# Kernel tuning notes

Hardware: AMD Instinct MI355X
Metric: run time of the kernel (lower is better)

Reference implementation:

```python
import jax, jax.numpy as jnp
import numpy as np
import math

KEY_DIM = 16
COMPAT_FACTOR = 1.0 / math.sqrt(KEY_DIM)


def setup_inputs() -> dict:
    key = jax.random.key(0)
    k1, k2, k3, k4, k5 = jax.random.split(key, 5)
    B, G, D, H, K, V = 4, 2048, 128, 8, 16, 16
    h = jax.random.normal(k1, (B, G, D), dtype=jnp.float32)
    # mask: 1 = masked-out (attention forced to zero), 0 = attend
    mask = jax.random.randint(k2, (G, G), 0, 2, dtype=jnp.int32)
    # xavier_uniform over (input_dim, key_dim) fan per head
    lim_qk = math.sqrt(6.0 / (D + K))
    lim_v = math.sqrt(6.0 / (D + V))
    W_Q = jax.random.uniform(k3, (H, D, K), jnp.float32, -lim_qk, lim_qk)
    W_K = jax.random.uniform(k4, (H, D, K), jnp.float32, -lim_qk, lim_qk)
    W_V = jax.random.uniform(k5, (H, D, V), jnp.float32, -lim_v, lim_v)
    return {"h": h, "mask": mask, "W_Q": W_Q, "W_K": W_K, "W_V": W_V}


def reference(h, mask, W_Q, W_K, W_V):
    # h: [B, G, D]; W_Q/W_K: [H, D, K]; W_V: [H, D, V]; mask: [G, G] (1 = masked)
    q = jnp.einsum("bgd,hdk->bhgk", h, W_Q)  # [B, H, G, K]
    k = jnp.einsum("bgd,hdk->bhgk", h, W_K)  # [B, H, G, K]
    v = jnp.einsum("bgd,hdv->bhgv", h, W_V)  # [B, H, G, V]
    compat = COMPAT_FACTOR * jnp.einsum("bhqk,bhgk->bhqg", q, k)  # [B, H, G, G]
    masked = (mask > 0)[None, None, :, :]  # broadcast over batch, heads
    neg = jnp.finfo(compat.dtype).min
    compat = jnp.where(masked, neg, compat)
    attn = jax.nn.softmax(compat, axis=-1)
    # post-softmax hard zeroing at masked positions (as in the original)
    attn = jnp.where(masked, jnp.zeros((), attn.dtype), attn)
    h_p = jnp.einsum("bhqg,bhgv->bhqv", attn, v)  # [B, H, G, V]
    return h_p
```

## Files before the change

### kernel.cpp

```cpp
#include <hip/hip_runtime.h>
#include <hip/hip_bf16.h>

#define GG 2048
#define DD 128
#define HH 8
#define BH 32

typedef _Float16 h2 __attribute__((ext_vector_type(2)));
typedef _Float16 h4 __attribute__((ext_vector_type(4)));
typedef _Float16 h8 __attribute__((ext_vector_type(8)));
typedef __attribute__((ext_vector_type(4))) float f32x4;
typedef unsigned short u16;
typedef unsigned int   u32;
typedef unsigned char  u8;
typedef unsigned long long u64;

#define QSCALE 0.36067376022224085f

#define OFF_Q  0u
#define OFF_KV (2u << 20)
#define OFF_M  (6u << 20)

#if __has_builtin(__builtin_amdgcn_exp2f)
#define EXP2F(x) __builtin_amdgcn_exp2f(x)
#else
#define EXP2F(x) exp2f(x)
#endif

#define MFMA16(a, b, c) __builtin_amdgcn_mfma_f32_16x16x16f16(a, b, c, 0, 0, 0)

static __device__ __forceinline__ u16 f16b(float x) {
  return __builtin_bit_cast(u16, (_Float16)x);
}

__global__ __launch_bounds__(256) void prep_kernel(
    const float* __restrict__ h, const int* __restrict__ mask,
    const float* __restrict__ WQ, const float* __restrict__ WK,
    const float* __restrict__ WV,
    _Float16* __restrict__ Qh, u8* __restrict__ KVp, u8* __restrict__ mbt)
{
  const int blk = blockIdx.x, tid = threadIdx.x;

  if (blk >= 256) {
    int t = (blk - 256) * 256 + tid;
    const int* m = mask + (size_t)t * 8;
    int4 m0 = *(const int4*)m;
    int4 m1 = *(const int4*)(m + 4);
    u32 byte = (m0.x > 0) | ((m0.y > 0) << 1) | ((m0.z > 0) << 2) | ((m0.w > 0) << 3)
             | ((m1.x > 0) << 4) | ((m1.y > 0) << 5) | ((m1.z > 0) << 6) | ((m1.w > 0) << 7);
    int q  = t >> 8;
    int k8 = t & 255;
    mbt[(size_t)(k8 >> 4) * (GG * 16) + (size_t)q * 16 + (k8 & 15)] = (u8)byte;
    return;
  }

  __shared__ _Float16 Wl[48 * 136];
  const int bh = blk >> 3, b = bh >> 3, hh = bh & (HH - 1);

  #pragma unroll
  for (int m = 0; m < 3; ++m) {
    const float* W = (m == 0 ? WQ : (m == 1 ? WK : WV)) + (size_t)hh * DD * 16;
    const float sc = (m == 0) ? QSCALE : 1.0f;
    #pragma unroll
    for (int i = 0; i < 2; ++i) {
      int j4 = i * 256 + tid;
      float4 v = ((const float4*)W)[j4];
      int j = j4 * 4, d = j >> 4, n0 = m * 16 + (j & 15);
      Wl[(n0 + 0) * 136 + d] = (_Float16)(v.x * sc);
      Wl[(n0 + 1) * 136 + d] = (_Float16)(v.y * sc);
      Wl[(n0 + 2) * 136 + d] = (_Float16)(v.z * sc);
      Wl[(n0 + 3) * 136 + d] = (_Float16)(v.w * sc);
    }
  }
  __syncthreads();

  const int wave = tid >> 6, lane = tid & 63;
  const int col = lane & 15, quad = lane >> 4;
  const int g0 = ((blk & 7) * 4 + wave) * 64;
  const float* hb = h + (size_t)b * GG * DD;

  f32x4 acc[4][3];
  #pragma unroll
  for (int mt = 0; mt < 4; ++mt)
    #pragma unroll
    for (int nt = 0; nt < 3; ++nt)
      acc[mt][nt] = (f32x4){0.f, 0.f, 0.f, 0.f};

  #pragma unroll
  for (int s = 0; s < 4; ++s) {
    h8 a[4], bw[3];
    #pragma unroll
    for (int mt = 0; mt < 4; ++mt) {
      const float* src = hb + (size_t)(g0 + mt * 16 + col) * DD + s * 32 + quad * 8;
      float4 x = ((const float4*)src)[0];
      float4 y = ((const float4*)src)[1];
      a[mt] = (h8){ (_Float16)x.x, (_Float16)x.y, (_Float16)x.z, (_Float16)x.w,
                    (_Float16)y.x, (_Float16)y.y, (_Float16)y.z, (_Float16)y.w };
    }
    #pragma unroll
    for (int nt = 0; nt < 3; ++nt)
      bw[nt] = *(const h8*)&Wl[(nt * 16 + col) * 136 + s * 32 + quad * 8];
    #pragma unroll
    for (int mt = 0; mt < 4; ++mt)
      #pragma unroll
      for (int nt = 0; nt < 3; ++nt)
        acc[mt][nt] = __builtin_amdgcn_mfma_f32_16x16x32_f16(a[mt], bw[nt], acc[mt][nt], 0, 0, 0);
  }

  u8* kvb = KVp + (size_t)bh * 16 * 8192;
  #pragma unroll
  for (int mt = 0; mt < 4; ++mt) {
    #pragma unroll
    for (int r = 0; r < 4; ++r) {
      int g = g0 + mt * 16 + quad * 4 + r;
      Qh[((size_t)bh * GG + g) * 16 + col] = (_Float16)acc[mt][0][r];
      int gi = g & 127;
      u8* tb = kvb + (size_t)(g >> 7) * 8192;
      *(u16*)(tb + gi * 32 + col * 2) = f16b(acc[mt][1][r]);
      *(u16*)(tb + 4096 + col * 256 + ((((gi >> 2) + col) & 31) * 8)
                 + (g & 3) * 2) = f16b(acc[mt][2][r]);
    }
  }
}

__global__ __launch_bounds__(512, 4) void attn_kernel(
    const _Float16* __restrict__ Qh, const u8* __restrict__ KVp,
    const u8* __restrict__ mbt, float* __restrict__ out)
{
  __shared__ __align__(16) u8 kv[2][16384];
  const int tid = threadIdx.x, wv = tid >> 6, lane = tid & 63;
  const int col = lane & 15, quad = lane >> 4;
  const int bh = blockIdx.x & 31;
  const int qb = (blockIdx.x >> 5) * 128 + wv * 16;

  const h4 qf = *(const h4*)(Qh + ((size_t)bh * GG + qb + col) * 16 + quad * 4);
  const u8* kvsrc = KVp + (size_t)bh * 16 * 8192;
  const u8* mrow  = mbt + (size_t)(qb + col) * 16;

  f32x4 acc = {0.f,0.f,0.f,0.f}, lacc = {0.f,0.f,0.f,0.f};
  const f32x4 cinit = {-4.f, -4.f, -4.f, -4.f};
  const h4 ones = {(_Float16)1.f, (_Float16)1.f, (_Float16)1.f, (_Float16)1.f};
  const int shq = quad * 4;

  auto tile = [&](const u8* cur, uint4 mv) {
    const _Float16* ldsK = (const _Float16*)cur;
    const u8* ldsV = cur + 4096;
    u64 w0 = ((u64)mv.x | ((u64)mv.y << 32)) >> shq;
    u64 w1 = ((u64)mv.z | ((u64)mv.w << 32)) >> shq;
    #pragma unroll
    for (int st = 0; st < 8; ++st) {
      h4 kf = *(const h4*)(ldsK + (size_t)(st * 16 + col) * 16 + quad * 4);
      h4 vf = *(const h4*)(ldsV + col * 256 + (((st * 4 + quad + col) & 31) * 8));

      f32x4 s = MFMA16(kf, qf, cinit);
      u32 bits = (u32)(((st < 4) ? w0 : w1) >> ((st & 3) * 16)) & 0xFu;
      float p0 = (bits & 1u) ? 0.f : EXP2F(s[0]);
      float p1 = (bits & 2u) ? 0.f : EXP2F(s[1]);
      float p2 = (bits & 4u) ? 0.f : EXP2F(s[2]);
      float p3 = (bits & 8u) ? 0.f : EXP2F(s[3]);

      h2 a01 = __builtin_bit_cast(h2, __builtin_amdgcn_cvt_pkrtz(p0, p1));
      h2 a23 = __builtin_bit_cast(h2, __builtin_amdgcn_cvt_pkrtz(p2, p3));
      h4 pf = __builtin_shufflevector(a01, a23, 0, 1, 2, 3);

      acc  = MFMA16(vf, pf, acc);
      lacc = MFMA16(ones, pf, lacc);
    }
  };

  {
    uint4 a0 = *(const uint4*)(kvsrc + tid * 32);
    uint4 a1 = *(const uint4*)(kvsrc + tid * 32 + 16);
    *(uint4*)(kv[0] + tid * 32) = a0;
    *(uint4*)(kv[0] + tid * 32 + 16) = a1;
  }
  uint4 mv0 = *(const uint4*)mrow;
  uint4 mv1 = *(const uint4*)(mrow + (size_t)(GG * 16));
  __syncthreads();

  for (int it = 0; it < 8; ++it) {
    uint4 na0, na1, nm0, nm1;
    if (it < 7) {
      const u8* ns = kvsrc + (size_t)(it + 1) * 16384 + tid * 32;
      na0 = *(const uint4*)ns;
      na1 = *(const uint4*)(ns + 16);
      nm0 = *(const uint4*)(mrow + (size_t)(2 * it + 2) * (GG * 16));
      nm1 = *(const uint4*)(mrow + (size_t)(2 * it + 3) * (GG * 16));
    }

    const u8* cur = kv[it & 1];
    tile(cur, mv0);
    tile(cur + 8192, mv1);

    if (it < 7) {
      u8* nb = kv[(it + 1) & 1];
      *(uint4*)(nb + tid * 32) = na0;
      *(uint4*)(nb + tid * 32 + 16) = na1;
      mv0 = nm0; mv1 = nm1;
      __syncthreads();
    }
  }

  const float l = lacc[0];
  const float rl = (l > 0.f) ? (1.f / l) : 0.f;
  float4 o = { acc[0] * rl, acc[1] * rl, acc[2] * rl, acc[3] * rl };
  *(float4*)(out + ((size_t)bh * GG + qb + col) * 16 + quad * 4) = o;
}

extern "C" void kernel_launch(void* const* d_in, const int* in_sizes, int n_in,
                              void* d_out, int out_size, void* d_ws, size_t ws_size,
                              hipStream_t stream) {
  const float* h    = (const float*)d_in[0];
  const int*   mask = (const int*)d_in[1];
  const float* WQ   = (const float*)d_in[2];
  const float* WK   = (const float*)d_in[3];
  const float* WV   = (const float*)d_in[4];
  float* out = (float*)d_out;
  char* ws = (char*)d_ws;
  _Float16* Qh  = (_Float16*)(ws + OFF_Q);
  u8*       KVp = (u8*)(ws + OFF_KV);
  u8*       mbt = (u8*)(ws + OFF_M);

  hipLaunchKernelGGL(prep_kernel, dim3(256 + GG * GG / (256 * 8)), dim3(256), 0, stream,
                     h, mask, WQ, WK, WV, Qh, KVp, mbt);
  hipLaunchKernelGGL(attn_kernel, dim3(BH * (GG / 128)), dim3(512), 0, stream,
                     Qh, KVp, mbt, out);
}
```

Before: 112.6 us.

## Split key range across wave halves with two query tiles per wave and LDS reduction

Each wave now handles 32 queries (two 16-row tiles) over half of the key range, and the two wave groups' partial numerators and denominators are combined through shared memory at the end. Each K/V fragment read from LDS is reused for two query tiles, which halves LDS reads per MFMA and gives more independent MFMA chains per wave. This adds LDS space for the reduction, an extra barrier, and more registers per thread, which may limit occupancy at the 512x4 launch bounds.

```diff
diff --git a/kernel.cpp b/kernel.cpp
--- a/kernel.cpp
+++ b/kernel.cpp
@@ -128,83 +128,127 @@
     const u8* __restrict__ mbt, float* __restrict__ out)
 {
   __shared__ __align__(16) u8 kv[2][16384];
+  __shared__ float Lacc[4][32][17];
+  __shared__ float Ll[4][32];
   const int tid = threadIdx.x, wv = tid >> 6, lane = tid & 63;
   const int col = lane & 15, quad = lane >> 4;
+  const int g  = wv & 3;
+  const int kh = wv >> 2;
   const int bh = blockIdx.x & 31;
-  const int qb = (blockIdx.x >> 5) * 128 + wv * 16;
-
-  const h4 qf = *(const h4*)(Qh + ((size_t)bh * GG + qb + col) * 16 + quad * 4);
+  const int qb = (blockIdx.x >> 5) * 128 + g * 32;
+
+  const h4 qf0 = *(const h4*)(Qh + ((size_t)bh * GG + qb + col) * 16 + quad * 4);
+  const h4 qf1 = *(const h4*)(Qh + ((size_t)bh * GG + qb + 16 + col) * 16 + quad * 4);
+
   const u8* kvsrc = KVp + (size_t)bh * 16 * 8192;
-  const u8* mrow  = mbt + (size_t)(qb + col) * 16;
-
-  f32x4 acc = {0.f,0.f,0.f,0.f}, lacc = {0.f,0.f,0.f,0.f};
+  const u8* mr0 = mbt + (size_t)(qb + col) * 16;
+  const u8* mr1 = mbt + (size_t)(qb + 16 + col) * 16;
+
+  f32x4 acc0 = {0.f,0.f,0.f,0.f}, acc1 = {0.f,0.f,0.f,0.f};
+  f32x4 lacc0 = {0.f,0.f,0.f,0.f}, lacc1 = {0.f,0.f,0.f,0.f};
   const f32x4 cinit = {-4.f, -4.f, -4.f, -4.f};
   const h4 ones = {(_Float16)1.f, (_Float16)1.f, (_Float16)1.f, (_Float16)1.f};
   const int shq = quad * 4;
 
-  auto tile = [&](const u8* cur, uint4 mv) {
+  const int sthalf = tid >> 8, sttid = tid & 255;
+
+  {
+    const u8* s0 = kvsrc + (size_t)(sthalf * 8) * 8192 + sttid * 32;
+    *(uint4*)(kv[0] + sthalf * 8192 + sttid * 32) = *(const uint4*)s0;
+    *(uint4*)(kv[0] + sthalf * 8192 + sttid * 32 + 16) = *(const uint4*)(s0 + 16);
+  }
+  const size_t tstep = (size_t)(GG * 16);
+  uint4 mv0 = *(const uint4*)(mr0 + (size_t)(kh * 8) * tstep);
+  uint4 mv1 = *(const uint4*)(mr1 + (size_t)(kh * 8) * tstep);
+  __syncthreads();
+
+  for (int it = 0; it < 8; ++it) {
+    uint4 ns0, ns1, nm0, nm1;
+    if (it < 7) {
+      const u8* ns = kvsrc + (size_t)(sthalf * 8 + it + 1) * 8192 + sttid * 32;
+      ns0 = *(const uint4*)ns;
+      ns1 = *(const uint4*)(ns + 16);
+      nm0 = *(const uint4*)(mr0 + (size_t)(kh * 8 + it + 1) * tstep);
+      nm1 = *(const uint4*)(mr1 + (size_t)(kh * 8 + it + 1) * tstep);
+    }
+
+    const u8* cur = kv[it & 1] + kh * 8192;
     const _Float16* ldsK = (const _Float16*)cur;
     const u8* ldsV = cur + 4096;
-    u64 w0 = ((u64)mv.x | ((u64)mv.y << 32)) >> shq;
-    u64 w1 = ((u64)mv.z | ((u64)mv.w << 32)) >> shq;
+    u64 wa0 = ((u64)mv0.x | ((u64)mv0.y << 32)) >> shq;
+    u64 wa1 = ((u64)mv0.z | ((u64)mv0.w << 32)) >> shq;
+    u64 wb0 = ((u64)mv1.x | ((u64)mv1.y << 32)) >> shq;
+    u64 wb1 = ((u64)mv1.z | ((u64)mv1.w << 32)) >> shq;
+
     #pragma unroll
     for (int st = 0; st < 8; ++st) {
       h4 kf = *(const h4*)(ldsK + (size_t)(st * 16 + col) * 16 + quad * 4);
       h4 vf = *(const h4*)(ldsV + col * 256 + (((st * 4 + quad + col) & 31) * 8));
 
-      f32x4 s = MFMA16(kf, qf, cinit);
-      u32 bits = (u32)(((st < 4) ? w0 : w1) >> ((st & 3) * 16)) & 0xFu;
-      float p0 = (bits & 1u) ? 0.f : EXP2F(s[0]);
-      float p1 = (bits & 2u) ? 0.f : EXP2F(s[1]);
-      float p2 = (bits & 4u) ? 0.f : EXP2F(s[2]);
-      float p3 = (bits & 8u) ? 0.f : EXP2F(s[3]);
-
-      h2 a01 = __builtin_bit_cast(h2, __builtin_amdgcn_cvt_pkrtz(p0, p1));
-      h2 a23 = __builtin_bit_cast(h2, __builtin_amdgcn_cvt_pkrtz(p2, p3));
-      h4 pf = __builtin_shufflevector(a01, a23, 0, 1, 2, 3);
-
-      acc  = MFMA16(vf, pf, acc);
-      lacc = MFMA16(ones, pf, lacc);
-    }
-  };
-
-  {
-    uint4 a0 = *(const uint4*)(kvsrc + tid * 32);
-    uint4 a1 = *(const uint4*)(kvsrc + tid * 32 + 16);
-    *(uint4*)(kv[0] + tid * 32) = a0;
-    *(uint4*)(kv[0] + tid * 32 + 16) = a1;
-  }
-  uint4 mv0 = *(const uint4*)mrow;
-  uint4 mv1 = *(const uint4*)(mrow + (size_t)(GG * 16));
-  __syncthreads();
-
-  for (int it = 0; it < 8; ++it) {
-    uint4 na0, na1, nm0, nm1;
+      f32x4 s0 = MFMA16(kf, qf0, cinit);
+      f32x4 s1 = MFMA16(kf, qf1, cinit);
+      const int sh = (st & 3) * 16;
+      u32 b0 = (u32)(((st < 4) ? wa0 : wa1) >> sh) & 0xFu;
+      u32 b1 = (u32)(((st < 4) ? wb0 : wb1) >> sh) & 0xFu;
+
+      float a0 = (b0 & 1u) ? 0.f : EXP2F(s0[0]);
+      float a1 = (b0 & 2u) ? 0.f : EXP2F(s0[1]);
+      float a2 = (b0 & 4u) ? 0.f : EXP2F(s0[2]);
+      float a3 = (b0 & 8u) ? 0.f : EXP2F(s0[3]);
+      float c0 = (b1 & 1u) ? 0.f : EXP2F(s1[0]);
+      float c1 = (b1 & 2u) ? 0.f : EXP2F(s1[1]);
+      float c2 = (b1 & 4u) ? 0.f : EXP2F(s1[2]);
+      float c3 = (b1 & 8u) ? 0.f : EXP2F(s1[3]);
+
+      h2 pa01 = __builtin_bit_cast(h2, __builtin_amdgcn_cvt_pkrtz(a0, a1));
+      h2 pa23 = __builtin_bit_cast(h2, __builtin_amdgcn_cvt_pkrtz(a2, a3));
+      h4 pf0 = __builtin_shufflevector(pa01, pa23, 0, 1, 2, 3);
+      h2 pc01 = __builtin_bit_cast(h2, __builtin_amdgcn_cvt_pkrtz(c0, c1));
+      h2 pc23 = __builtin_bit_cast(h2, __builtin_amdgcn_cvt_pkrtz(c2, c3));
+      h4 pf1 = __builtin_shufflevector(pc01, pc23, 0, 1, 2, 3);
+
+      acc0  = MFMA16(vf, pf0, acc0);
+      acc1  = MFMA16(vf, pf1, acc1);
+      lacc0 = MFMA16(ones, pf0, lacc0);
+      lacc1 = MFMA16(ones, pf1, lacc1);
+    }
+
     if (it < 7) {
-      const u8* ns = kvsrc + (size_t)(it + 1) * 16384 + tid * 32;
-      na0 = *(const uint4*)ns;
-      na1 = *(const uint4*)(ns + 16);
-      nm0 = *(const uint4*)(mrow + (size_t)(2 * it + 2) * (GG * 16));
-      nm1 = *(const uint4*)(mrow + (size_t)(2 * it + 3) * (GG * 16));
-    }
-
-    const u8* cur = kv[it & 1];
-    tile(cur, mv0);
-    tile(cur + 8192, mv1);
-
-    if (it < 7) {
-      u8* nb = kv[(it + 1) & 1];
-      *(uint4*)(nb + tid * 32) = na0;
-      *(uint4*)(nb + tid * 32 + 16) = na1;
+      u8* nb = kv[(it + 1) & 1] + sthalf * 8192;
+      *(uint4*)(nb + sttid * 32) = ns0;
+      *(uint4*)(nb + sttid * 32 + 16) = ns1;
       mv0 = nm0; mv1 = nm1;
       __syncthreads();
     }
   }
 
-  const float l = lacc[0];
-  const float rl = (l > 0.f) ? (1.f / l) : 0.f;
-  float4 o = { acc[0] * rl, acc[1] * rl, acc[2] * rl, acc[3] * rl };
-  *(float4*)(out + ((size_t)bh * GG + qb + col) * 16 + quad * 4) = o;
+  const float l0 = lacc0[0], l1 = lacc1[0];
+  if (kh == 0) {
+    #pragma unroll
+    for (int r = 0; r < 4; ++r) {
+      Lacc[g][col][shq + r]      = acc0[r];
+      Lacc[g][col + 16][shq + r] = acc1[r];
+    }
+    if (quad == 0) { Ll[g][col] = l0; Ll[g][col + 16] = l1; }
+  }
+  __syncthreads();
+  if (kh == 1) {
+    float la = Ll[g][col] + l0;
+    float lb = Ll[g][col + 16] + l1;
+    float ra = (la > 0.f) ? (1.f / la) : 0.f;
+    float rb = (lb > 0.f) ? (1.f / lb) : 0.f;
+    float4 o0, o1;
+    o0.x = (Lacc[g][col][shq + 0] + acc0[0]) * ra;
+    o0.y = (Lacc[g][col][shq + 1] + acc0[1]) * ra;
+    o0.z = (Lacc[g][col][shq + 2] + acc0[2]) * ra;
+    o0.w = (Lacc[g][col][shq + 3] + acc0[3]) * ra;
+    o1.x = (Lacc[g][col + 16][shq + 0] + acc1[0]) * rb;
+    o1.y = (Lacc[g][col + 16][shq + 1] + acc1[1]) * rb;
+    o1.z = (Lacc[g][col + 16][shq + 2] + acc1[2]) * rb;
+    o1.w = (Lacc[g][col + 16][shq + 3] + acc1[3]) * rb;
+    *(float4*)(out + ((size_t)bh * GG + qb + col) * 16 + shq) = o0;
+    *(float4*)(out + ((size_t)bh * GG + qb + 16 + col) * 16 + shq) = o1;
+  }
 }
 
 extern "C" void kernel_launch(void* const* d_in, const int* in_sizes, int n_in,
```

After: 107.8 us. -4.3%, faster.

## Split key range across two wave groups per block and fold mask into MFMA bias

Applied to the files above, without the earlier changes.

Attention blocks grow to 1024 threads. Waves 0-7 process the first half of the key tiles and waves 8-15 the second half, and the partial numerators and denominators are combined through shared memory at the end. The mask is now applied by seeding the QK MFMA accumulator with a large negative bias instead of selecting after exp2. This doubles wave-level parallelism per query tile, which should help latency hiding, at the cost of an extra reduction, more LDS, and occupancy limits from the larger block.

```diff
diff --git a/kernel.cpp b/kernel.cpp
--- a/kernel.cpp
+++ b/kernel.cpp
@@ -123,41 +123,66 @@
   }
 }
 
-__global__ __launch_bounds__(512, 4) void attn_kernel(
+__global__ __launch_bounds__(1024, 8) void attn_kernel(
     const _Float16* __restrict__ Qh, const u8* __restrict__ KVp,
     const u8* __restrict__ mbt, float* __restrict__ out)
 {
   __shared__ __align__(16) u8 kv[2][16384];
+  __shared__ float Lacc[8][16][17];
+  __shared__ float Ll[8][16];
   const int tid = threadIdx.x, wv = tid >> 6, lane = tid & 63;
   const int col = lane & 15, quad = lane >> 4;
+  const int qt = wv & 7;
+  const int kh = wv >> 3;
   const int bh = blockIdx.x & 31;
-  const int qb = (blockIdx.x >> 5) * 128 + wv * 16;
+  const int qb = (blockIdx.x >> 5) * 128 + qt * 16;
 
   const h4 qf = *(const h4*)(Qh + ((size_t)bh * GG + qb + col) * 16 + quad * 4);
   const u8* kvsrc = KVp + (size_t)bh * 16 * 8192;
   const u8* mrow  = mbt + (size_t)(qb + col) * 16;
 
   f32x4 acc = {0.f,0.f,0.f,0.f}, lacc = {0.f,0.f,0.f,0.f};
-  const f32x4 cinit = {-4.f, -4.f, -4.f, -4.f};
   const h4 ones = {(_Float16)1.f, (_Float16)1.f, (_Float16)1.f, (_Float16)1.f};
   const int shq = quad * 4;
 
-  auto tile = [&](const u8* cur, uint4 mv) {
+  const int sh2 = tid >> 9, stid = tid & 511;
+
+  *(uint4*)(kv[0] + sh2 * 8192 + stid * 16) =
+      *(const uint4*)(kvsrc + (size_t)(sh2 * 8) * 8192 + stid * 16);
+  const size_t tstep = (size_t)(GG * 16);
+  uint4 mv = *(const uint4*)(mrow + (size_t)(kh * 8) * tstep);
+  __syncthreads();
+
+  for (int it = 0; it < 8; ++it) {
+    uint4 ns, nm;
+    if (it < 7) {
+      ns = *(const uint4*)(kvsrc + (size_t)(sh2 * 8 + it + 1) * 8192 + stid * 16);
+      nm = *(const uint4*)(mrow + (size_t)(kh * 8 + it + 1) * tstep);
+    }
+
+    const u8* cur = kv[it & 1] + kh * 8192;
     const _Float16* ldsK = (const _Float16*)cur;
     const u8* ldsV = cur + 4096;
     u64 w0 = ((u64)mv.x | ((u64)mv.y << 32)) >> shq;
     u64 w1 = ((u64)mv.z | ((u64)mv.w << 32)) >> shq;
+
     #pragma unroll
     for (int st = 0; st < 8; ++st) {
       h4 kf = *(const h4*)(ldsK + (size_t)(st * 16 + col) * 16 + quad * 4);
       h4 vf = *(const h4*)(ldsV + col * 256 + (((st * 4 + quad + col) & 31) * 8));
 
-      f32x4 s = MFMA16(kf, qf, cinit);
       u32 bits = (u32)(((st < 4) ? w0 : w1) >> ((st & 3) * 16)) & 0xFu;
-      float p0 = (bits & 1u) ? 0.f : EXP2F(s[0]);
-      float p1 = (bits & 2u) ? 0.f : EXP2F(s[1]);
-      float p2 = (bits & 4u) ? 0.f : EXP2F(s[2]);
-      float p3 = (bits & 8u) ? 0.f : EXP2F(s[3]);
+      f32x4 cm;
+      cm[0] = (bits & 1u) ? -3000.f : -4.f;
+      cm[1] = (bits & 2u) ? -3000.f : -4.f;
+      cm[2] = (bits & 4u) ? -3000.f : -4.f;
+      cm[3] = (bits & 8u) ? -3000.f : -4.f;
+
+      f32x4 s = MFMA16(kf, qf, cm);
+      float p0 = EXP2F(s[0]);
+      float p1 = EXP2F(s[1]);
+      float p2 = EXP2F(s[2]);
+      float p3 = EXP2F(s[3]);
 
       h2 a01 = __builtin_bit_cast(h2, __builtin_amdgcn_cvt_pkrtz(p0, p1));
       h2 a23 = __builtin_bit_cast(h2, __builtin_amdgcn_cvt_pkrtz(p2, p3));
@@ -166,45 +191,31 @@
       acc  = MFMA16(vf, pf, acc);
       lacc = MFMA16(ones, pf, lacc);
     }
-  };
-
-  {
-    uint4 a0 = *(const uint4*)(kvsrc + tid * 32);
-    uint4 a1 = *(const uint4*)(kvsrc + tid * 32 + 16);
-    *(uint4*)(kv[0] + tid * 32) = a0;
-    *(uint4*)(kv[0] + tid * 32 + 16) = a1;
-  }
-  uint4 mv0 = *(const uint4*)mrow;
-  uint4 mv1 = *(const uint4*)(mrow + (size_t)(GG * 16));
+
+    if (it < 7) {
+      *(uint4*)(kv[(it + 1) & 1] + sh2 * 8192 + stid * 16) = ns;
+      mv = nm;
+      __syncthreads();
+    }
+  }
+
+  const float l = lacc[0];
+  if (kh == 0) {
+    #pragma unroll
+    for (int r = 0; r < 4; ++r) Lacc[qt][col][shq + r] = acc[r];
+    if (quad == 0) Ll[qt][col] = l;
+  }
   __syncthreads();
-
-  for (int it = 0; it < 8; ++it) {
-    uint4 na0, na1, nm0, nm1;
-    if (it < 7) {
-      const u8* ns = kvsrc + (size_t)(it + 1) * 16384 + tid * 32;
-      na0 = *(const uint4*)ns;
-      na1 = *(const uint4*)(ns + 16);
-      nm0 = *(const uint4*)(mrow + (size_t)(2 * it + 2) * (GG * 16));
-      nm1 = *(const uint4*)(mrow + (size_t)(2 * it + 3) * (GG * 16));
-    }
-
-    const u8* cur = kv[it & 1];
-    tile(cur, mv0);
-    tile(cur + 8192, mv1);
-
-    if (it < 7) {
-      u8* nb = kv[(it + 1) & 1];
-      *(uint4*)(nb + tid * 32) = na0;
-      *(uint4*)(nb + tid * 32 + 16) = na1;
-      mv0 = nm0; mv1 = nm1;
-      __syncthreads();
-    }
-  }
-
-  const float l = lacc[0];
-  const float rl = (l > 0.f) ? (1.f / l) : 0.f;
-  float4 o = { acc[0] * rl, acc[1] * rl, acc[2] * rl, acc[3] * rl };
-  *(float4*)(out + ((size_t)bh * GG + qb + col) * 16 + quad * 4) = o;
+  if (kh == 1) {
+    float la = Ll[qt][col] + l;
+    float ra = (la > 0.f) ? (1.f / la) : 0.f;
+    float4 o;
+    o.x = (Lacc[qt][col][shq + 0] + acc[0]) * ra;
+    o.y = (Lacc[qt][col][shq + 1] + acc[1]) * ra;
+    o.z = (Lacc[qt][col][shq + 2] + acc[2]) * ra;
+    o.w = (Lacc[qt][col][shq + 3] + acc[3]) * ra;
+    *(float4*)(out + ((size_t)bh * GG + qb + col) * 16 + shq) = o;
+  }
 }
 
 extern "C" void kernel_launch(void* const* d_in, const int* in_sizes, int n_in,
@@ -223,6 +234,6 @@
 
   hipLaunchKernelGGL(prep_kernel, dim3(256 + GG * GG / (256 * 8)), dim3(256), 0, stream,
                      h, mask, WQ, WK, WV, Qh, KVp, mbt);
-  hipLaunchKernelGGL(attn_kernel, dim3(BH * (GG / 128)), dim3(512), 0, stream,
+  hipLaunchKernelGGL(attn_kernel, dim3(BH * (GG / 128)), dim3(1024), 0, stream,
                      Qh, KVp, mbt, out);
 }
```

New measurement: 107.4 us. 4.6% less time.
